# Performance work log

Hardware: AMD Instinct MI355X
Metric: run time of the kernel (lower is better)

The kernel has to match this reference:

```python
import jax, jax.numpy as jnp
import numpy as np
from jax import lax

ALPHA = 0.6
BETA = 0.4
GROUP = 22   # players per match (fixed group size)
TOPK = 11    # dream11 team size; min(11, 22) == 11
M = 500_000  # number of match groups
N = M * GROUP


def setup_inputs() -> dict:
    key = jax.random.key(0)
    k1, k2 = jax.random.split(key)
    pred = jax.random.normal(k1, (N,), dtype=jnp.float32)
    target = jax.random.normal(k2, (N,), dtype=jnp.float32)
    # contiguous equal-size groups: [0,0,...,0, 1,1,...,1, ...]
    batch_ids = jnp.repeat(jnp.arange(M, dtype=jnp.int64), GROUP)
    return {"pred": pred, "target": target, "batch_ids": batch_ids}


def _overlap_penalty(p, t):
    # p, t: [M, GROUP]
    m = p.shape[0]
    _, pi = lax.top_k(p, TOPK)  # [M, TOPK] indices within group
    _, ti = lax.top_k(t, TOPK)
    rows = jnp.arange(m)[:, None]
    pm = jnp.zeros((m, GROUP), dtype=bool).at[rows, pi].set(True)
    tm = jnp.zeros((m, GROUP), dtype=bool).at[rows, ti].set(True)
    overlap = jnp.sum(pm & tm, axis=-1)  # [M] set-intersection size
    penalty = 1.0 - overlap.astype(p.dtype) / TOPK
    return jnp.mean(penalty)


def reference(pred, target, batch_ids):
    mse = jnp.mean((pred - target) ** 2)
    # batch_ids are sorted contiguous equal-size groups of GROUP rows
    m = pred.shape[0] // GROUP
    p = pred.reshape(m, GROUP)
    t = target.reshape(m, GROUP)
    overlap_loss = _overlap_penalty(p, t)
    return ALPHA * mse + BETA * overlap_loss
```

## Files before the change

### kernel.cpp

```cpp
#include <hip/hip_runtime.h>

#define ALPHA_C 0.6f
#define BETA_C  0.4f
#define GROUP_C 22
#define TOPK_C  11
#define BLOCK_C 256
#define NEG_BIG (-3.0e38f)


__device__ __forceinline__ void ce_desc(float& x, float& y) {
    float hi = fmaxf(x, y);
    float lo = fminf(x, y);
    x = hi; y = lo;
}

template<int I, int END, int R, int M>
struct MLoop {
    static __device__ __forceinline__ void run(float* a) {
        if constexpr (I + R < END) {
            ce_desc(a[I], a[I + R]);
            MLoop<I + M, END, R, M>::run(a);
        }
    }
};

template<int LO, int N, int R>
struct Merge {
    static __device__ __forceinline__ void run(float* a) {
        constexpr int M = R * 2;
        if constexpr (M < N) {
            Merge<LO, N, M>::run(a);
            Merge<LO + R, N, M>::run(a);
            MLoop<LO + R, LO + N, R, M>::run(a);
        } else {
            ce_desc(a[LO], a[LO + R]);
        }
    }
};

template<int LO, int N>
struct Sort {
    static __device__ __forceinline__ void run(float* a) {
        if constexpr (N > 1) {
            Sort<LO, N / 2>::run(a);
            Sort<LO + N / 2, N / 2>::run(a);
            Merge<LO, N, 1>::run(a);
        }
    }
};

__device__ __forceinline__ float sel11_of_22(const float* v) {
    float A[16], B[8];
#pragma unroll
    for (int i = 0; i < 16; ++i) A[i] = v[i];
#pragma unroll
    for (int i = 0; i < 6; ++i) B[i] = v[16 + i];
    B[6] = NEG_BIG; B[7] = NEG_BIG;
    Sort<0, 16>::run(A);
    Sort<0, 8>::run(B);
    float thr = A[10];
    thr = fmaxf(thr, fminf(A[9], B[0]));
    thr = fmaxf(thr, fminf(A[8], B[1]));
    thr = fmaxf(thr, fminf(A[7], B[2]));
    thr = fmaxf(thr, fminf(A[6], B[3]));
    thr = fmaxf(thr, fminf(A[5], B[4]));
    thr = fmaxf(thr, fminf(A[4], B[5]));
    return thr;
}

__global__ __launch_bounds__(BLOCK_C, 4) void ol_main(
    const float* __restrict__ pred, const float* __restrict__ target,
    int M, float* __restrict__ ws_s, float* __restrict__ ws_o)
{
    int g = blockIdx.x * BLOCK_C + threadIdx.x;
    float s = 0.0f;
    int ov = 0;

    if (g < M) {
        float p[GROUP_C], t[GROUP_C];
        const float2* gp = (const float2*)(pred + (size_t)g * GROUP_C);
        const float2* gt = (const float2*)(target + (size_t)g * GROUP_C);
#pragma unroll
        for (int j = 0; j < GROUP_C / 2; ++j) {
            float2 v = gp[j]; p[2 * j] = v.x; p[2 * j + 1] = v.y;
            float2 w = gt[j]; t[2 * j] = w.x; t[2 * j + 1] = w.y;
        }

        float thr_p = sel11_of_22(p);
        float thr_t = sel11_of_22(t);

#pragma unroll
        for (int j = 0; j < GROUP_C; ++j) {
            float d = p[j] - t[j];
            s = fmaf(d, d, s);
            ov += (p[j] >= thr_p && t[j] >= thr_t) ? 1 : 0;
        }
    }

    float fov = (float)ov;
#pragma unroll
    for (int off = 32; off > 0; off >>= 1) {
        s   += __shfl_down(s, off);
        fov += __shfl_down(fov, off);
    }

    __shared__ float sm_s[BLOCK_C / 64];
    __shared__ float sm_o[BLOCK_C / 64];
    int lane = threadIdx.x & 63;
    int wid  = threadIdx.x >> 6;
    if (lane == 0) { sm_s[wid] = s; sm_o[wid] = fov; }
    __syncthreads();

    if (threadIdx.x == 0) {
        float ss = sm_s[0] + sm_s[1] + sm_s[2] + sm_s[3];
        float oo = sm_o[0] + sm_o[1] + sm_o[2] + sm_o[3];
        ws_s[blockIdx.x] = ss;
        ws_o[blockIdx.x] = oo;
    }
}

__global__ __launch_bounds__(BLOCK_C) void ol_finalize(
    const float* __restrict__ ws_s, const float* __restrict__ ws_o,
    int nblocks, float* __restrict__ out, int M)
{
    float s = 0.0f, o = 0.0f;
    for (int i = threadIdx.x; i < nblocks; i += BLOCK_C) {
        s += ws_s[i];
        o += ws_o[i];
    }
#pragma unroll
    for (int off = 32; off > 0; off >>= 1) {
        s += __shfl_down(s, off);
        o += __shfl_down(o, off);
    }
    __shared__ float sm_s[BLOCK_C / 64];
    __shared__ float sm_o[BLOCK_C / 64];
    int lane = threadIdx.x & 63;
    int wid  = threadIdx.x >> 6;
    if (lane == 0) { sm_s[wid] = s; sm_o[wid] = o; }
    __syncthreads();
    if (threadIdx.x == 0) {
        float ss = sm_s[0] + sm_s[1] + sm_s[2] + sm_s[3];
        float oo = sm_o[0] + sm_o[1] + sm_o[2] + sm_o[3];
        float n   = (float)M * (float)GROUP_C;
        float mse = ss / n;
        float pen = 1.0f - oo / ((float)TOPK_C * (float)M);
        out[0] = ALPHA_C * mse + BETA_C * pen;
    }
}

extern "C" void kernel_launch(void* const* d_in, const int* in_sizes, int n_in,
                              void* d_out, int out_size, void* d_ws, size_t ws_size,
                              hipStream_t stream) {
    const float* pred   = (const float*)d_in[0];
    const float* target = (const float*)d_in[1];

    int N = in_sizes[0];
    int M = N / GROUP_C;
    int blocks = (M + BLOCK_C - 1) / BLOCK_C;

    float* ws_s = (float*)d_ws;
    float* ws_o = ws_s + blocks;

    hipLaunchKernelGGL(ol_main, dim3(blocks), dim3(BLOCK_C), 0, stream,
                       pred, target, M, ws_s, ws_o);
    hipLaunchKernelGGL(ol_finalize, dim3(1), dim3(BLOCK_C), 0, stream,
                       ws_s, ws_o, blocks, (float*)d_out, M);
}
```

Measured before the change: 142.8 us.

## Stage group data through LDS with coalesced float4 loads

Each block now loads its contiguous slab of pred and target into shared memory using coalesced float4 loads, then each thread reads its 22-element group from LDS. Before, every thread read its group directly with strided float2 loads (88-byte stride across lanes), which coalesces poorly. In exchange the kernel uses about 45 KB of LDS per block, which may limit occupancy below the launch-bounds target, and the stride-22 LDS reads may cause bank conflicts.

```diff
diff --git a/kernel.cpp b/kernel.cpp
--- a/kernel.cpp
+++ b/kernel.cpp
@@ -5,6 +5,8 @@
 #define GROUP_C 22
 #define TOPK_C  11
 #define BLOCK_C 256
+#define GRP_PER_BLK 256
+#define FLT_PER_BLK (GRP_PER_BLK * GROUP_C)
 #define NEG_BIG (-3.0e38f)
 
 
@@ -72,18 +74,46 @@
     const float* __restrict__ pred, const float* __restrict__ target,
     int M, float* __restrict__ ws_s, float* __restrict__ ws_o)
 {
-    int g = blockIdx.x * BLOCK_C + threadIdx.x;
+    __shared__ __align__(16) float smp[FLT_PER_BLK];
+    __shared__ __align__(16) float smt[FLT_PER_BLK];
+
+    const int tid = threadIdx.x;
+    const size_t base_f = (size_t)blockIdx.x * FLT_PER_BLK;
+    const int rem_g = min(GRP_PER_BLK, M - blockIdx.x * GRP_PER_BLK);
+    const int rem_f = rem_g * GROUP_C;
+    const int nf4 = rem_f >> 2;
+
+    const float4* gp4 = (const float4*)(pred + base_f);
+    const float4* gt4 = (const float4*)(target + base_f);
+#pragma unroll
+    for (int k = 0; k < (FLT_PER_BLK / 4 + BLOCK_C - 1) / BLOCK_C; ++k) {
+        int idx = k * BLOCK_C + tid;
+        if (idx < nf4) {
+            float4 v = gp4[idx];
+            *((float4*)&smp[idx * 4]) = v;
+            float4 w = gt4[idx];
+            *((float4*)&smt[idx * 4]) = w;
+        }
+    }
+    if ((rem_f & 3) && tid == 0) {
+        const float2* g2p = (const float2*)(pred + base_f);
+        const float2* g2t = (const float2*)(target + base_f);
+        ((float2*)smp)[nf4 * 2] = g2p[nf4 * 2];
+        ((float2*)smt)[nf4 * 2] = g2t[nf4 * 2];
+    }
+    __syncthreads();
+
     float s = 0.0f;
     int ov = 0;
 
-    if (g < M) {
+    if (tid < rem_g) {
         float p[GROUP_C], t[GROUP_C];
-        const float2* gp = (const float2*)(pred + (size_t)g * GROUP_C);
-        const float2* gt = (const float2*)(target + (size_t)g * GROUP_C);
+        const float2* lp = (const float2*)&smp[tid * GROUP_C];
+        const float2* lt = (const float2*)&smt[tid * GROUP_C];
 #pragma unroll
         for (int j = 0; j < GROUP_C / 2; ++j) {
-            float2 v = gp[j]; p[2 * j] = v.x; p[2 * j + 1] = v.y;
-            float2 w = gt[j]; t[2 * j] = w.x; t[2 * j + 1] = w.y;
+            float2 v = lp[j]; p[2 * j] = v.x; p[2 * j + 1] = v.y;
+            float2 w = lt[j]; t[2 * j] = w.x; t[2 * j + 1] = w.y;
         }
 
         float thr_p = sel11_of_22(p);
@@ -106,12 +136,12 @@
 
     __shared__ float sm_s[BLOCK_C / 64];
     __shared__ float sm_o[BLOCK_C / 64];
-    int lane = threadIdx.x & 63;
-    int wid  = threadIdx.x >> 6;
+    int lane = tid & 63;
+    int wid  = tid >> 6;
     if (lane == 0) { sm_s[wid] = s; sm_o[wid] = fov; }
     __syncthreads();
 
-    if (threadIdx.x == 0) {
+    if (tid == 0) {
         float ss = sm_s[0] + sm_s[1] + sm_s[2] + sm_s[3];
         float oo = sm_o[0] + sm_o[1] + sm_o[2] + sm_o[3];
         ws_s[blockIdx.x] = ss;
@@ -157,7 +187,7 @@
 
     int N = in_sizes[0];
     int M = N / GROUP_C;
-    int blocks = (M + BLOCK_C - 1) / BLOCK_C;
+    int blocks = (M + GRP_PER_BLK - 1) / GRP_PER_BLK;
 
     float* ws_s = (float*)d_ws;
     float* ws_o = ws_s + blocks;
```

Measured after the change: 144.6 us. Within noise of the previous version (+1.3%).

## Stage per-wave group data through LDS with coalesced float4 loads

Applied to the files above, without the earlier changes.

Each wave now loads its 64 groups of pred and target cooperatively as contiguous float4 chunks into shared memory, and each lane then reads its own 22-element row from LDS. This replaces strided per-thread float2 global loads, which touch many cache lines per wave instruction, with fully coalesced loads. The block-level shared reduction and __syncthreads are removed by writing one partial sum per wave, so the finalize kernel reduces four times as many slots. The cost is about 45 KB of LDS per block, which may limit occupancy, plus possible LDS bank conflicts on the 22-float row reads.

```diff
diff --git a/kernel.cpp b/kernel.cpp
--- a/kernel.cpp
+++ b/kernel.cpp
@@ -5,6 +5,9 @@
 #define GROUP_C 22
 #define TOPK_C  11
 #define BLOCK_C 256
+#define WAVES_PB (BLOCK_C / 64)
+#define WAVE_G 64
+#define WAVE_F (WAVE_G * GROUP_C)
 #define NEG_BIG (-3.0e38f)
 
 
@@ -72,28 +75,57 @@
     const float* __restrict__ pred, const float* __restrict__ target,
     int M, float* __restrict__ ws_s, float* __restrict__ ws_o)
 {
-    int g = blockIdx.x * BLOCK_C + threadIdx.x;
+    __shared__ __align__(16) float smp[WAVES_PB][WAVE_F];
+    __shared__ __align__(16) float smt[WAVES_PB][WAVE_F];
+
+    const int tid  = threadIdx.x;
+    const int lane = tid & 63;
+    const int wid  = tid >> 6;
+
+    const int wave_g0 = blockIdx.x * BLOCK_C + wid * WAVE_G;
+    const int rem_g   = min(WAVE_G, M - wave_g0);
+
     float s = 0.0f;
     int ov = 0;
 
-    if (g < M) {
-        float p[GROUP_C], t[GROUP_C];
-        const float2* gp = (const float2*)(pred + (size_t)g * GROUP_C);
-        const float2* gt = (const float2*)(target + (size_t)g * GROUP_C);
+    if (rem_g > 0) {
+        const int rem_f = rem_g * GROUP_C;
+        const int nch   = rem_f >> 2;
+        const size_t base_f = (size_t)wave_g0 * GROUP_C;
+        const float4* gp4 = (const float4*)(pred + base_f);
+        const float4* gt4 = (const float4*)(target + base_f);
+        float* lp = smp[wid];
+        float* lt = smt[wid];
 #pragma unroll
-        for (int j = 0; j < GROUP_C / 2; ++j) {
-            float2 v = gp[j]; p[2 * j] = v.x; p[2 * j + 1] = v.y;
-            float2 w = gt[j]; t[2 * j] = w.x; t[2 * j + 1] = w.y;
+        for (int k = 0; k < (WAVE_F / 4 + 63) / 64; ++k) {
+            int idx = k * 64 + lane;
+            if (idx < nch) {
+                float4 v = gp4[idx];
+                *((float4*)&lp[idx * 4]) = v;
+                float4 w = gt4[idx];
+                *((float4*)&lt[idx * 4]) = w;
+            }
         }
 
-        float thr_p = sel11_of_22(p);
-        float thr_t = sel11_of_22(t);
+        if (lane < rem_g) {
+            float p[GROUP_C], t[GROUP_C];
+            const float2* rp = (const float2*)&lp[lane * GROUP_C];
+            const float2* rt = (const float2*)&lt[lane * GROUP_C];
+#pragma unroll
+            for (int j = 0; j < GROUP_C / 2; ++j) {
+                float2 v = rp[j]; p[2 * j] = v.x; p[2 * j + 1] = v.y;
+                float2 w = rt[j]; t[2 * j] = w.x; t[2 * j + 1] = w.y;
+            }
+
+            float thr_p = sel11_of_22(p);
+            float thr_t = sel11_of_22(t);
 
 #pragma unroll
-        for (int j = 0; j < GROUP_C; ++j) {
-            float d = p[j] - t[j];
-            s = fmaf(d, d, s);
-            ov += (p[j] >= thr_p && t[j] >= thr_t) ? 1 : 0;
+            for (int j = 0; j < GROUP_C; ++j) {
+                float d = p[j] - t[j];
+                s = fmaf(d, d, s);
+                ov += (p[j] >= thr_p && t[j] >= thr_t) ? 1 : 0;
+            }
         }
     }
 
@@ -103,28 +135,19 @@
         s   += __shfl_down(s, off);
         fov += __shfl_down(fov, off);
     }
-
-    __shared__ float sm_s[BLOCK_C / 64];
-    __shared__ float sm_o[BLOCK_C / 64];
-    int lane = threadIdx.x & 63;
-    int wid  = threadIdx.x >> 6;
-    if (lane == 0) { sm_s[wid] = s; sm_o[wid] = fov; }
-    __syncthreads();
-
-    if (threadIdx.x == 0) {
-        float ss = sm_s[0] + sm_s[1] + sm_s[2] + sm_s[3];
-        float oo = sm_o[0] + sm_o[1] + sm_o[2] + sm_o[3];
-        ws_s[blockIdx.x] = ss;
-        ws_o[blockIdx.x] = oo;
+    if (lane == 0) {
+        int wslot = blockIdx.x * WAVES_PB + wid;
+        ws_s[wslot] = s;
+        ws_o[wslot] = fov;
     }
 }
 
 __global__ __launch_bounds__(BLOCK_C) void ol_finalize(
     const float* __restrict__ ws_s, const float* __restrict__ ws_o,
-    int nblocks, float* __restrict__ out, int M)
+    int nslots, float* __restrict__ out, int M)
 {
     float s = 0.0f, o = 0.0f;
-    for (int i = threadIdx.x; i < nblocks; i += BLOCK_C) {
+    for (int i = threadIdx.x; i < nslots; i += BLOCK_C) {
         s += ws_s[i];
         o += ws_o[i];
     }
@@ -158,12 +181,13 @@
     int N = in_sizes[0];
     int M = N / GROUP_C;
     int blocks = (M + BLOCK_C - 1) / BLOCK_C;
+    int nslots = blocks * WAVES_PB;
 
     float* ws_s = (float*)d_ws;
-    float* ws_o = ws_s + blocks;
+    float* ws_o = ws_s + nslots;
 
     hipLaunchKernelGGL(ol_main, dim3(blocks), dim3(BLOCK_C), 0, stream,
                        pred, target, M, ws_s, ws_o);
     hipLaunchKernelGGL(ol_finalize, dim3(1), dim3(BLOCK_C), 0, stream,
-                       ws_s, ws_o, blocks, (float*)d_out, M);
+                       ws_s, ws_o, nslots, (float*)d_out, M);
 }
```

Result: slower. 151.0 us (+5.8%).
